# Optimization experiments

Measured on AMD Instinct MI355X. Metric: run time of the kernel, lower is better.

## Reference

```python
import jax, jax.numpy as jnp
import numpy as np

D_MODEL = 2048
NUM_HEADS = 16
HEAD_DIM = 128


def setup_inputs() -> dict:
    key = jax.random.key(0)
    ks = jax.random.split(key, 9)
    B, S = 2, 2048
    s_in = 1.0 / np.sqrt(D_MODEL)
    return {
        "x": jax.random.normal(ks[0], (B, S, D_MODEL), dtype=jnp.float32),
        "wq": jax.random.normal(ks[1], (D_MODEL, D_MODEL), dtype=jnp.float32) * s_in,
        "bq": jnp.zeros((D_MODEL,), jnp.float32),
        "wk": jax.random.normal(ks[2], (D_MODEL, HEAD_DIM), dtype=jnp.float32) * s_in,
        "bk": jnp.zeros((HEAD_DIM,), jnp.float32),
        "wv": jax.random.normal(ks[3], (D_MODEL, HEAD_DIM), dtype=jnp.float32) * s_in,
        "bv": jnpp_zeros(ks) if False else jnp.zeros((HEAD_DIM,), jnp.float32),
        "wo": jax.random.normal(ks[4], (D_MODEL, D_MODEL), dtype=jnp.float32) * s_in,
        "bo": jnp.zeros((D_MODEL,), jnp.float32),
    }


def reference(x, wq, bq, wk, bk, wv, bv, wo, bo):
    B, S, _ = x.shape
    H, Dh = NUM_HEADS, HEAD_DIM
    q = (x @ wq + bq).reshape(B, S, H, Dh)          # [B,S,H,Dh]
    k = x @ wk + bk                                  # [B,S,Dh] (single KV head)
    v = x @ wv + bv                                  # [B,S,Dh]
    scale = 1.0 / jnp.sqrt(jnp.asarray(Dh, x.dtype))
    # scores: [B,H,Sq,Sk] — MQA: K shared across heads
    scores = jnp.einsum('bqhd,bkd->bhqk', q, k) * scale
    attn = jax.nn.softmax(scores, axis=-1)
    out = jnp.einsum('bhqk,bkd->bqhd', attn, v).reshape(B, S, H * Dh)
    return out @ wo + bo
```

## Files before the change

### kernel.cpp

```cpp
#include <hip/hip_runtime.h>
#include <stdint.h>

typedef unsigned short u16;

#define D_MODEL 2048
#define HEADS 16
#define HDIM 128
#define SEQ 2048
#define BATCH 2
#define NROWS (BATCH*SEQ)
#define QKV_N (D_MODEL + 2*HDIM)

#define SC2F 0.12751743f

typedef __attribute__((ext_vector_type(8))) short bf16x8;
typedef __attribute__((ext_vector_type(4))) float f32x4;

__device__ inline u16 f2bf(float f) {
  union { float f; uint32_t u; } v; v.f = f;
  uint32_t r = v.u + 0x7FFFu + ((v.u >> 16) & 1u);
  return (u16)(r >> 16);
}
__device__ inline u16 f2bf_fast(float f) {
  union { float f; uint32_t u; } v; v.f = f;
  return (u16)((v.u + 0x8000u) >> 16);
}

__device__ inline void gload_lds16(const void* g, void* l) {
  __builtin_amdgcn_global_load_lds(
      (const __attribute__((address_space(1))) unsigned int*)g,
      (__attribute__((address_space(3))) unsigned int*)l, 16, 0, 0);
}

__global__ void prep_all(const float* __restrict__ x, u16* __restrict__ xb,
                         const float* __restrict__ wq, const float* __restrict__ wk,
                         const float* __restrict__ wv, const float* __restrict__ wo,
                         u16* __restrict__ wqkvT, u16* __restrict__ woT,
                         const float* __restrict__ bq, const float* __restrict__ bk,
                         const float* __restrict__ bv, float* __restrict__ biasq) {
  const int bid = blockIdx.x, tid = threadIdx.x;
  if (bid < 1024) {
    const float4* xf = (const float4*)x;
    ushort4* xo = (ushort4*)xb;
    int i = bid * 256 + tid;
#pragma unroll
    for (int r = 0; r < 8; r++, i += 262144) {
      float4 f = xf[i];
      ushort4 u;
      u.x = f2bf(f.x); u.y = f2bf(f.y); u.z = f2bf(f.z); u.w = f2bf(f.w);
      xo[i] = u;
    }
  } else if (bid < 9728) {
    __shared__ float t[32][33];
    const int b2 = bid - 1024;
    const int n0v = (b2 % 136) * 32, k0 = (b2 / 136) * 32;
    const float* src; int N, n0, drow; u16* dst; float scl = 1.0f;
    if (n0v < 2048)      { src = wq; N = 2048; n0 = n0v;        dst = wqkvT; drow = n0v; scl = SC2F; }
    else if (n0v < 2176) { src = wk; N = 128;  n0 = n0v - 2048; dst = wqkvT; drow = n0v; }
    else if (n0v < 2304) { src = wv; N = 128;  n0 = n0v - 2176; dst = wqkvT; drow = n0v; }
    else                 { src = wo; N = 2048; n0 = n0v - 2304; dst = woT;   drow = n0v - 2304; }
    const int tx = tid & 31, ty = tid >> 5;
#pragma unroll
    for (int i = 0; i < 4; i++)
      t[ty + 8*i][tx] = src[(size_t)(k0 + ty + 8*i) * N + n0 + tx];
    __syncthreads();
#pragma unroll
    for (int i = 0; i < 4; i++)
      dst[(size_t)(drow + ty + 8*i) * D_MODEL + k0 + tx] = f2bf(t[tx][ty + 8*i] * scl);
  } else {
    for (int i = tid; i < QKV_N; i += 256)
      biasq[i] = (i < D_MODEL) ? bq[i] * SC2F
               : ((i < D_MODEL + HDIM) ? bk[i - D_MODEL] : bv[i - D_MODEL - HDIM]);
  }
}

#define BM2 256
#define BN2 256
#define BKK 64

__global__ __launch_bounds__(512, 2) void gemm256(
    const u16* __restrict__ A, const u16* __restrict__ BT,
    const float* __restrict__ bias,
    u16* __restrict__ Cb, float* __restrict__ Cf,
    u16* __restrict__ vT,
    int M, int N, int tilesN, int K) {
  __shared__ __align__(16) u16 sA[2][BM2 * BKK];
  __shared__ __align__(16) u16 sB[2][BN2 * BKK];
  const int tid = threadIdx.x;
  const int wave = tid >> 6, lane = tid & 63;
  const int bm = blockIdx.x / tilesN, bn = blockIdx.x % tilesN;
  const int m0 = bm * BM2, n0 = bn * BN2;
  const int wm = (wave >> 2) * 128, wn = (wave & 3) * 64;
  const int l16 = lane & 15, quad = lane >> 4;

  f32x4 acc[8][4] = {};

  const int dRow = lane >> 3;
  const int dCol = ((lane & 7) ^ (lane >> 3)) * 8;

#define GDMA2(i, buf)                                                          \
  {                                                                            \
    const int _k0 = (i) * BKK;                                                 \
    _Pragma("unroll") for (int c = 0; c < 4; c++) {                            \
      const int op = wave * 4 + c;                                             \
      const int row = op * 8 + dRow;                                           \
      gload_lds16(&A[(size_t)(m0 + row) * K + _k0 + dCol], &sA[buf][op * 512]);\
      gload_lds16(&BT[(size_t)(n0 + row) * K + _k0 + dCol], &sB[buf][op * 512]);\
    }                                                                          \
  }

  const int NI = K / BKK;
  GDMA2(0, 0);
  for (int i = 0; i < NI; i++) {
    const int cur = i & 1;
    __syncthreads();
    if (i + 1 < NI) GDMA2(i + 1, cur ^ 1);
#pragma unroll
    for (int kk2 = 0; kk2 < 2; kk2++) {
      bf16x8 bfr[4];
#pragma unroll
      for (int nb = 0; nb < 4; ++nb) {
        const int R = wn + nb * 16 + l16;
        const int s = (kk2 * 4 + quad) ^ (l16 & 7);
        bfr[nb] = *(const bf16x8*)&sB[cur][R * BKK + s * 8];
      }
#pragma unroll
      for (int mb = 0; mb < 8; ++mb) {
        const int R = wm + mb * 16 + l16;
        const int s = (kk2 * 4 + quad) ^ (l16 & 7);
        bf16x8 af = *(const bf16x8*)&sA[cur][R * BKK + s * 8];
#pragma unroll
        for (int nb = 0; nb < 4; ++nb)
          acc[mb][nb] = __builtin_amdgcn_mfma_f32_16x16x32_bf16(af, bfr[nb], acc[mb][nb], 0, 0, 0);
      }
    }
  }
#undef GDMA2

#pragma unroll
  for (int mb = 0; mb < 8; ++mb) {
#pragma unroll
    for (int nb = 0; nb < 4; ++nb) {
      const int gn = n0 + wn + nb * 16 + l16;
      const float bb = bias ? bias[gn] : 0.0f;
#pragma unroll
      for (int r = 0; r < 4; ++r) {
        const int gm = m0 + wm + mb * 16 + quad * 4 + r;
        const float v = acc[mb][nb][r] + bb;
        if (Cf) {
          Cf[(size_t)gm * N + gn] = v;
        } else {
          const u16 u = f2bf(v);
          Cb[(size_t)gm * N + gn] = u;
          if (vT && gn >= D_MODEL + HDIM) {
            const int bi = gm >> 11, si = gm & 2047;
            vT[((size_t)bi * HDIM + (gn - D_MODEL - HDIM)) * SEQ + si] = u;
          }
        }
      }
    }
  }
}

__global__ __launch_bounds__(256) void mqa_attn(
    const u16* __restrict__ qkv, const u16* __restrict__ vT, u16* __restrict__ ctx) {
  __shared__ __align__(16) u16 sK[2][64 * 128];
  __shared__ __align__(16) u16 sV[128 * 64];
  __shared__ __align__(16) u16 sP[4][32 * 64];
  const int tid = threadIdx.x, wave = tid >> 6, lane = tid & 63;
  const int qt = blockIdx.x & 15;
  const int h  = (blockIdx.x >> 4) & 15;
  const int b  = blockIdx.x >> 8;
  const int bS = b * SEQ;
  const int q0 = qt * 128 + wave * 32;
  const int l16 = lane & 15, quad = lane >> 4;
  const int sw = l16 & 7;
  u16* myP = &sP[wave][0];

  bf16x8 qf[2][4];
#pragma unroll
  for (int mb = 0; mb < 2; mb++)
#pragma unroll
    for (int kc = 0; kc < 4; kc++)
      qf[mb][kc] = *(const bf16x8*)&qkv[(size_t)(bS + q0 + mb*16 + l16) * QKV_N
                                        + h*HDIM + kc*32 + quad*8];

  f32x4 o[2][8] = {};
  float lrow[2] = {0.f, 0.f};

  const u16* Kbase = qkv + (size_t)bS * QKV_N + D_MODEL;
  const u16* Vbase = vT + (size_t)b * HDIM * SEQ;

  const int kRowIn = lane >> 4;
  const int kChS   = lane & 15;
  const int vRowIn = lane >> 3;
  const int vChL   = (lane & 7) ^ (lane >> 3);

#define DMA_K(t, dst)                                                          \
  {                                                                            \
    const int _sk = (t) * 64;                                                  \
    _Pragma("unroll") for (int j = 0; j < 4; j++) {                            \
      const int i = wave * 4 + j;                                              \
      const int krow = i * 4 + kRowIn;                                         \
      const int kcl = kChS ^ (krow & 15);                                      \
      gload_lds16(&Kbase[(size_t)(_sk + krow) * QKV_N + kcl * 8],              \
                  &(dst)[i * 512]);                                            \
    }                                                                          \
  }
#define DMA_V(t)                                                               \
  {                                                                            \
    const int _sk = (t) * 64;                                                  \
    _Pragma("unroll") for (int j = 0; j < 4; j++) {                            \
      const int i = wave * 4 + j;                                              \
      const int d = i * 8 + vRowIn;                                            \
      gload_lds16(&Vbase[(size_t)d * SEQ + _sk + vChL * 8], &sV[i * 512]);     \
    }                                                                          \
  }

  DMA_K(0, sK[0]);
  DMA_V(0);
  __syncthreads();

  const int T = SEQ / 64;
  for (int t = 0; t < T; ++t) {
    const int cur = t & 1;
    if (t + 1 < T) DMA_K(t + 1, sK[cur ^ 1]);

    f32x4 sc[2][4];
#pragma unroll
    for (int nb = 0; nb < 4; nb++) {
      bf16x8 kf[4];
#pragma unroll
      for (int kc = 0; kc < 4; kc++)
        kf[kc] = *(const bf16x8*)&sK[cur][(nb*16 + l16) * 128 + (((kc*4 + quad) ^ l16) * 8)];
#pragma unroll
      for (int mb = 0; mb < 2; mb++) {
        f32x4 a = {0.f, 0.f, 0.f, 0.f};
#pragma unroll
        for (int kc = 0; kc < 4; kc++)
          a = __builtin_amdgcn_mfma_f32_16x16x32_bf16(kf[kc], qf[mb][kc], a, 0, 0, 0);
        sc[mb][nb] = a;
      }
    }

#pragma unroll
    for (int mb = 0; mb < 2; mb++)
#pragma unroll
      for (int nb = 0; nb < 4; nb++) {
        float p0 = __builtin_amdgcn_exp2f(sc[mb][nb][0]);
        float p1 = __builtin_amdgcn_exp2f(sc[mb][nb][1]);
        float p2 = __builtin_amdgcn_exp2f(sc[mb][nb][2]);
        float p3 = __builtin_amdgcn_exp2f(sc[mb][nb][3]);
        lrow[mb] += (p0 + p1) + (p2 + p3);
        uint32_t lo = (uint32_t)f2bf_fast(p0) | ((uint32_t)f2bf_fast(p1) << 16);
        uint32_t hi = (uint32_t)f2bf_fast(p2) | ((uint32_t)f2bf_fast(p3) << 16);
        uint2 w; w.x = lo; w.y = hi;
        const int pr = (nb*2 + (quad >> 1)) ^ sw;
        *(uint2*)&myP[(mb*16 + l16) * 64 + pr * 8 + (quad & 1) * 4] = w;
      }

    __syncthreads();

    bf16x8 pf[2][2];
#pragma unroll
    for (int mb = 0; mb < 2; mb++)
#pragma unroll
      for (int kc = 0; kc < 2; kc++)
        pf[mb][kc] = *(const bf16x8*)&myP[(mb*16 + l16) * 64 + (((kc*4 + quad) ^ sw) * 8)];

#pragma unroll
    for (int nb = 0; nb < 8; nb++) {
      bf16x8 vf[2];
#pragma unroll
      for (int kc = 0; kc < 2; kc++)
        vf[kc] = *(const bf16x8*)&sV[(nb*16 + l16) * 64 + (((kc*4 + quad) ^ (l16 & 7)) * 8)];
#pragma unroll
      for (int mb = 0; mb < 2; mb++)
#pragma unroll
        for (int kc = 0; kc < 2; kc++)
          o[mb][nb] = __builtin_amdgcn_mfma_f32_16x16x32_bf16(pf[mb][kc], vf[kc], o[mb][nb], 0, 0, 0);
    }

    __syncthreads();
    if (t + 1 < T) DMA_V(t + 1);
  }

#pragma unroll
  for (int mb = 0; mb < 2; mb++) {
    lrow[mb] += __shfl_xor(lrow[mb], 16, 64);
    lrow[mb] += __shfl_xor(lrow[mb], 32, 64);
  }
  float invl[2][4];
#pragma unroll
  for (int mb = 0; mb < 2; mb++)
#pragma unroll
    for (int r = 0; r < 4; r++)
      invl[mb][r] = 1.0f / __shfl(lrow[mb], quad * 4 + r, 64);

#pragma unroll
  for (int mb = 0; mb < 2; mb++)
#pragma unroll
    for (int nb = 0; nb < 8; nb++)
#pragma unroll
      for (int r = 0; r < 4; r++) {
        const int gq = q0 + mb*16 + quad*4 + r;
        const int gd = h * HDIM + nb*16 + l16;
        ctx[(size_t)(bS + gq) * D_MODEL + gd] = f2bf(o[mb][nb][r] * invl[mb][r]);
      }
}

extern "C" void kernel_launch(void* const* d_in, const int* in_sizes, int n_in,
                              void* d_out, int out_size, void* d_ws, size_t ws_size,
                              hipStream_t stream) {
  const float* x  = (const float*)d_in[0];
  const float* wq = (const float*)d_in[1];
  const float* bq = (const float*)d_in[2];
  const float* wk = (const float*)d_in[3];
  const float* bk = (const float*)d_in[4];
  const float* wv = (const float*)d_in[5];
  const float* bv = (const float*)d_in[6];
  const float* wo = (const float*)d_in[7];
  const float* bo = (const float*)d_in[8];
  float* out = (float*)d_out;
  char* ws = (char*)d_ws;

  u16*   xb    = (u16*)(ws + 0);
  u16*   wqkvT = (u16*)(ws + 16777216);
  u16*   woT   = (u16*)(ws + 26214400);
  u16*   qkv   = (u16*)(ws + 34603008);
  u16*   vT    = (u16*)(ws + 53477376);
  u16*   ctx   = (u16*)(ws + 54525952);
  float* biasq = (float*)(ws + 71303168);

  prep_all<<<9729, 256, 0, stream>>>(x, xb, wq, wk, wv, wo, wqkvT, woT,
                                     bq, bk, bv, biasq);
  gemm256<<<16 * 9, 512, 0, stream>>>(xb, wqkvT, biasq, qkv, nullptr, vT,
                                      NROWS, QKV_N, 9, D_MODEL);
  mqa_attn<<<BATCH * HEADS * (SEQ / 128), 256, 0, stream>>>(qkv, vT, ctx);
  gemm256<<<16 * 8, 512, 0, stream>>>(ctx, woT, bo, nullptr, out, nullptr,
                                      NROWS, D_MODEL, 8, D_MODEL);
}
```

Measured before the change: 348.8 us.

## Interleave GEMM tile prefetch with MFMA steps and remap blocks across XCDs

The bf16 GEMM is rewritten so that the loads for the next K-tile are spread across the eight per-row MFMA sub-steps. Fine-grained vmcnt waits and a barrier at each step replace the single coarse sync per tile, and s_setprio is raised around the MFMA bursts. Block indices are also remapped so consecutive output tiles land on the same XCD, which is meant to improve L2 reuse. The aim is to hide global-to-LDS latency behind compute, at the cost of more barriers and hand-tuned waitcnt logic that depends on the order loads are issued.

```diff
diff --git a/kernel.cpp b/kernel.cpp
--- a/kernel.cpp
+++ b/kernel.cpp
@@ -74,23 +74,23 @@
   }
 }
 
-#define BM2 256
-#define BN2 256
-#define BKK 64
-
-__global__ __launch_bounds__(512, 2) void gemm256(
+#define NXCD 8
+
+__global__ __launch_bounds__(512, 2) void gemm256p(
     const u16* __restrict__ A, const u16* __restrict__ BT,
     const float* __restrict__ bias,
     u16* __restrict__ Cb, float* __restrict__ Cf,
     u16* __restrict__ vT,
     int M, int N, int tilesN, int K) {
-  __shared__ __align__(16) u16 sA[2][BM2 * BKK];
-  __shared__ __align__(16) u16 sB[2][BN2 * BKK];
+  __shared__ __align__(16) u16 sA[2][256 * 64];
+  __shared__ __align__(16) u16 sB[2][256 * 64];
   const int tid = threadIdx.x;
   const int wave = tid >> 6, lane = tid & 63;
-  const int bm = blockIdx.x / tilesN, bn = blockIdx.x % tilesN;
-  const int m0 = bm * BM2, n0 = bn * BN2;
-  const int wm = (wave >> 2) * 128, wn = (wave & 3) * 64;
+  const int nwg = gridDim.x, cpx = nwg / NXCD;
+  const int rb = (blockIdx.x % NXCD) * cpx + blockIdx.x / NXCD;
+  const int bm = rb / tilesN, bn = rb % tilesN;
+  const int m0 = bm * 256, n0 = bn * 256;
+  const int wmi = wave >> 2, wni = wave & 3;
   const int l16 = lane & 15, quad = lane >> 4;
 
   f32x4 acc[8][4] = {};
@@ -98,54 +98,72 @@
   const int dRow = lane >> 3;
   const int dCol = ((lane & 7) ^ (lane >> 3)) * 8;
 
-#define GDMA2(i, buf)                                                          \
-  {                                                                            \
-    const int _k0 = (i) * BKK;                                                 \
-    _Pragma("unroll") for (int c = 0; c < 4; c++) {                            \
-      const int op = wave * 4 + c;                                             \
-      const int row = op * 8 + dRow;                                           \
-      gload_lds16(&A[(size_t)(m0 + row) * K + _k0 + dCol], &sA[buf][op * 512]);\
-      gload_lds16(&BT[(size_t)(n0 + row) * K + _k0 + dCol], &sB[buf][op * 512]);\
-    }                                                                          \
-  }
-
-  const int NI = K / BKK;
-  GDMA2(0, 0);
-  for (int i = 0; i < NI; i++) {
-    const int cur = i & 1;
-    __syncthreads();
-    if (i + 1 < NI) GDMA2(i + 1, cur ^ 1);
-#pragma unroll
-    for (int kk2 = 0; kk2 < 2; kk2++) {
-      bf16x8 bfr[4];
-#pragma unroll
-      for (int nb = 0; nb < 4; ++nb) {
-        const int R = wn + nb * 16 + l16;
-        const int s = (kk2 * 4 + quad) ^ (l16 & 7);
-        bfr[nb] = *(const bf16x8*)&sB[cur][R * BKK + s * 8];
-      }
-#pragma unroll
-      for (int mb = 0; mb < 8; ++mb) {
-        const int R = wm + mb * 16 + l16;
-        const int s = (kk2 * 4 + quad) ^ (l16 & 7);
-        bf16x8 af = *(const bf16x8*)&sA[cur][R * BKK + s * 8];
+#define STAGE_B(tt, c)                                                         \
+  { const int op = wave * 4 + (c); const int row = op * 8 + dRow;              \
+    gload_lds16(&BT[(size_t)(n0 + row) * K + (tt) * 64 + dCol],                \
+                &sB[(tt) & 1][op * 512]); }
+#define STAGE_A(tt, c)                                                         \
+  { const int op = wave * 4 + (c); const int row = op * 8 + dRow;              \
+    gload_lds16(&A[(size_t)(m0 + row) * K + (tt) * 64 + dCol],                 \
+                &sA[(tt) & 1][op * 512]); }
+
+  STAGE_B(0, 0); STAGE_B(0, 1); STAGE_B(0, 2); STAGE_B(0, 3);
+  STAGE_A(0, 0); STAGE_A(0, 1); STAGE_A(0, 2); STAGE_A(0, 3);
+
+  const int NT = K / 64;
+  for (int t = 0; t < NT; ++t) {
+    const int cur = t & 1;
+    bf16x8 bfr[4][2];
+#pragma unroll
+    for (int p = 0; p < 8; ++p) {
+      if (p == 0) asm volatile("s_waitcnt vmcnt(2)" ::: "memory");
+      if (p == 1) {
+        if (t + 1 < NT) asm volatile("s_waitcnt vmcnt(1)" ::: "memory");
+        else            asm volatile("s_waitcnt vmcnt(0)" ::: "memory");
+      }
+      __builtin_amdgcn_s_barrier();
+      if (p == 0) {
 #pragma unroll
         for (int nb = 0; nb < 4; ++nb)
-          acc[mb][nb] = __builtin_amdgcn_mfma_f32_16x16x32_bf16(af, bfr[nb], acc[mb][nb], 0, 0, 0);
-      }
-    }
-  }
-#undef GDMA2
+#pragma unroll
+          for (int kk = 0; kk < 2; ++kk) {
+            const int R = wni * 64 + nb * 16 + l16;
+            const int s = (kk * 4 + quad) ^ (l16 & 7);
+            bfr[nb][kk] = *(const bf16x8*)&sB[cur][R * 64 + s * 8];
+          }
+      }
+      bf16x8 af[2];
+#pragma unroll
+      for (int kk = 0; kk < 2; ++kk) {
+        const int R = wmi * 128 + p * 16 + l16;
+        const int s = (kk * 4 + quad) ^ (l16 & 7);
+        af[kk] = *(const bf16x8*)&sA[cur][R * 64 + s * 8];
+      }
+      if (t + 1 < NT) {
+        if (p < 4) { STAGE_B(t + 1, p); }
+        else       { STAGE_A(t + 1, p - 4); }
+      }
+      __builtin_amdgcn_s_setprio(1);
+#pragma unroll
+      for (int kk = 0; kk < 2; ++kk)
+#pragma unroll
+        for (int nb = 0; nb < 4; ++nb)
+          acc[p][nb] = __builtin_amdgcn_mfma_f32_16x16x32_bf16(af[kk], bfr[nb][kk], acc[p][nb], 0, 0, 0);
+      __builtin_amdgcn_s_setprio(0);
+    }
+  }
+#undef STAGE_A
+#undef STAGE_B
 
 #pragma unroll
   for (int mb = 0; mb < 8; ++mb) {
 #pragma unroll
     for (int nb = 0; nb < 4; ++nb) {
-      const int gn = n0 + wn + nb * 16 + l16;
+      const int gn = n0 + wni * 64 + nb * 16 + l16;
       const float bb = bias ? bias[gn] : 0.0f;
 #pragma unroll
       for (int r = 0; r < 4; ++r) {
-        const int gm = m0 + wm + mb * 16 + quad * 4 + r;
+        const int gm = m0 + wmi * 128 + mb * 16 + quad * 4 + r;
         const float v = acc[mb][nb][r] + bb;
         if (Cf) {
           Cf[(size_t)gm * N + gn] = v;
@@ -334,9 +352,9 @@
 
   prep_all<<<9729, 256, 0, stream>>>(x, xb, wq, wk, wv, wo, wqkvT, woT,
                                      bq, bk, bv, biasq);
-  gemm256<<<16 * 9, 512, 0, stream>>>(xb, wqkvT, biasq, qkv, nullptr, vT,
-                                      NROWS, QKV_N, 9, D_MODEL);
+  gemm256p<<<16 * 9, 512, 0, stream>>>(xb, wqkvT, biasq, qkv, nullptr, vT,
+                                       NROWS, QKV_N, 9, D_MODEL);
   mqa_attn<<<BATCH * HEADS * (SEQ / 128), 256, 0, stream>>>(qkv, vT, ctx);
-  gemm256<<<16 * 8, 512, 0, stream>>>(ctx, woT, bo, nullptr, out, nullptr,
-                                      NROWS, D_MODEL, 8, D_MODEL);
-}
+  gemm256p<<<16 * 8, 512, 0, stream>>>(ctx, woT, bo, nullptr, out, nullptr,
+                                       NROWS, D_MODEL, 8, D_MODEL);
+}
```

Measured after the change: 389.9 us. 11.8% more time.
